# Performance work log

Hardware: AMD Instinct MI355X
Metric: run time of the kernel (lower is better)

The kernel has to match this reference:

```python
import jax, jax.numpy as jnp
import numpy as np
from jax.ops import segment_sum

N_NODES = 100000
N_EDGES = 1600000
N_GRAPHS = 128


def setup_inputs() -> dict:
    key = jax.random.key(0)
    ks = jax.random.split(key, 16)
    x = jax.random.normal(ks[0], (N_NODES, 128), dtype=jnp.float32)
    edge_index = jax.random.randint(ks[1], (2, N_EDGES), 0, N_NODES, dtype=jnp.int64)
    batch = jnp.sort(jax.random.randint(ks[2], (N_NODES,), 0, N_GRAPHS, dtype=jnp.int64))
    def glorot(k, fan_in, fan_out):
        lim = (6.0 / (fan_in + fan_out)) ** 0.5
        return jax.random.uniform(k, (fan_in, fan_out), jnp.float32, -lim, lim)
    return {
        "x": x, "edge_index": edge_index, "batch": batch,
        "W1": glorot(ks[3], 128, 64), "b1": jnp.zeros((64,), jnp.float32),
        "W2": glorot(ks[4], 64, 64),  "b2": jnp.zeros((64,), jnp.float32),
        "W3": glorot(ks[5], 64, 64),  "b3": jnp.zeros((64,), jnp.float32),
        "W4": glorot(ks[6], 64, 64),  "b4": jnp.zeros((64,), jnp.float32),
        "Wl": glorot(ks[7], 64, 1),   "bl": jnp.zeros((1,), jnp.float32),
    }


def _gcn_layer(x, row, col, norm, W, b):
    # x: [N, Cin] -> [N, Cout]; gather source feats, scale, scatter-add at target
    h = x @ W                                 # dense transform first (GCNConv order)
    msg = norm[:, None] * h[row]              # [E, Cout]
    out = segment_sum(msg, col, num_segments=N_NODES)
    return out + b


def reference(x, edge_index, batch, W1, b1, W2, b2, W3, b3, W4, b4, Wl, bl):
    row, col = edge_index[0], edge_index[1]
    # symmetric degree normalization based on in-degree of col (PyG degree(col))
    deg = segment_sum(jnp.ones((N_EDGES,), x.dtype), col, num_segments=N_NODES)
    dinv = jnp.where(deg > 0, deg ** -0.5, jnp.zeros_like(deg))
    norm = dinv[row] * dinv[col]              # [E]

    h = _gcn_layer(x, row, col, norm, W1, b1)
    h = _gcn_layer(h, row, col, norm, W2, b2)
    h = _gcn_layer(h, row, col, norm, W3, b3)
    h = _gcn_layer(h, row, col, norm, W4, b4)  # [N, 64]

    # to_dense_batch + mean(dim=1): padded zeros count, so divide by max graph size
    sums = segment_sum(h, batch, num_segments=N_GRAPHS)          # [B, 64]
    counts = segment_sum(jnp.ones((N_NODES,), h.dtype), batch, num_segments=N_GRAPHS)
    n_max = jnp.max(counts)
    pooled = sums / n_max                                        # [B, 64]
    return pooled @ Wl + bl                                      # [B, 1]
```

## Files before the change

### kernel.cpp

```cpp
#include <hip/hip_runtime.h>
#include <hip/hip_bf16.h>
#include <hip/hip_fp16.h>

#define N_NODES 100000
#define N_EDGES 1600000
#define N_GRAPHS 128

#define BSH 9
#define BNODES 512
#define NB 196
#define CAP 12288
#define BLK 512
#define EPB (N_EDGES / BLK)
#define RECMAX 10240

#define SPLIT 4

typedef __attribute__((ext_vector_type(8))) _Float16 v8h;
typedef __attribute__((ext_vector_type(4))) float v4f;


__global__ __launch_bounds__(256) void k_hist(const int* __restrict__ col,
                                              int* __restrict__ hist_t) {
    __shared__ int h[NB];
    const int t = threadIdx.x, b = blockIdx.x;
    for (int i = t; i < NB; i += 256) h[i] = 0;
    __syncthreads();
    const int e0 = b * EPB;
    for (int i = t; i < EPB; i += 256) atomicAdd(&h[col[e0 + i] >> BSH], 1);
    __syncthreads();
    for (int i = t; i < NB; i += 256) hist_t[i * BLK + b] = h[i];
}

__global__ __launch_bounds__(512) void k_cursors(const int* __restrict__ hist_t,
                                                 int* __restrict__ cursors,
                                                 int* __restrict__ bcnt) {
    __shared__ int s[BLK];
    const int t = threadIdx.x, bin = blockIdx.x;
    const int v = hist_t[bin * BLK + t];
    s[t] = v; __syncthreads();
    for (int off = 1; off < BLK; off <<= 1) {
        int a = (t >= off) ? s[t - off] : 0;
        __syncthreads(); s[t] += a; __syncthreads();
    }
    cursors[bin * BLK + t] = bin * CAP + s[t] - v;
    if (t == BLK - 1) bcnt[bin] = s[t];
}

__global__ __launch_bounds__(256) void k_mid(const int* __restrict__ row,
                                             const int* __restrict__ col,
                                             const int* __restrict__ cursors,
                                             int* __restrict__ bedges) {
    __shared__ int cur[NB];
    const int t = threadIdx.x, b = blockIdx.x;
    for (int i = t; i < NB; i += 256) cur[i] = cursors[i * BLK + b];
    __syncthreads();
    const int e0 = b * EPB;
    for (int i = t; i < EPB; i += 256) {
        const int c = col[e0 + i];
        const int r = row[e0 + i];
        const int pos = atomicAdd(&cur[c >> BSH], 1);
        bedges[pos] = r | ((c & (BNODES - 1)) << 17);
    }
}

__global__ __launch_bounds__(512) void k_build(const int* __restrict__ bedges,
                                               const int* __restrict__ bcnt,
                                               int* __restrict__ csr,
                                               int* __restrict__ offs,
                                               int* __restrict__ deg_c,
                                               float* __restrict__ dinv) {
    __shared__ int rec[RECMAX];
    __shared__ int deg[BNODES];
    __shared__ int offx[BNODES];
    __shared__ int cur[BNODES];
    const int t = threadIdx.x, bin = blockIdx.x;
    const int base = bin * CAP;
    const int cnt = bcnt[bin];
    const int vb = bin << BSH;
    const int nn = min(BNODES, N_NODES - vb);
    for (int i = t; i < cnt; i += 512) rec[i] = bedges[base + i];
    deg[t] = 0;
    __syncthreads();
    for (int i = t; i < cnt; i += 512) atomicAdd(&deg[(rec[i] >> 17) & (BNODES - 1)], 1);
    __syncthreads();
    const int d = (t < nn) ? deg[t] : 0;
    const int pd = (d + 7) & ~7;
    offx[t] = pd; __syncthreads();
    for (int off = 1; off < BNODES; off <<= 1) {
        int a = (t >= off) ? offx[t - off] : 0;
        __syncthreads(); offx[t] += a; __syncthreads();
    }
    const int myoff = offx[t] - pd;
    cur[t] = myoff;
    if (t < nn) {
        offs[vb + t] = base + myoff;
        deg_c[vb + t] = d;
        dinv[vb + t] = (d > 0) ? rsqrtf((float)d) : 0.0f;
        for (int j = d; j < pd; j++) csr[base + myoff + j] = N_NODES;
    }
    __syncthreads();
    for (int i = t; i < cnt; i += 512) {
        const int r = rec[i];
        const int pos = atomicAdd(&cur[(r >> 17) & (BNODES - 1)], 1);
        csr[base + pos] = r & 0x1FFFF;
    }
}


template <int CIN>
__global__ __launch_bounds__(256) void k_gemm(const float* __restrict__ X,
                                              const float* __restrict__ W,
                                              const float* __restrict__ dinv,
                                              __half* __restrict__ H16) {
    constexpr int SA = 72;
    constexpr int SB = 72;
    __shared__ __align__(16) _Float16 sA[128 * SA];
    __shared__ __align__(16) _Float16 sBh[64 * SB];
    __shared__ __align__(16) _Float16 sBl[64 * SB];
    const int t = threadIdx.x;
    const int w = t >> 6, lane = t & 63;
    const int quad = lane >> 4, l16 = lane & 15;
    const int nb = blockIdx.x * 128;

    v4f acc[2][4] = {};

    for (int k0 = 0; k0 < CIN; k0 += 64) {
        if (k0) __syncthreads();
        for (int i = t; i < 64 * 16; i += 256) {
            const int k = i >> 4, c4 = (i & 15) * 4;
            const float4 wv = *reinterpret_cast<const float4*>(W + (size_t)(k0 + k) * 64 + c4);
            const float wf[4] = {wv.x, wv.y, wv.z, wv.w};
            #pragma unroll
            for (int j = 0; j < 4; j++) {
                const _Float16 hi = (_Float16)wf[j];
                sBh[(c4 + j) * SB + k] = hi;
                sBl[(c4 + j) * SB + k] = (_Float16)(wf[j] - (float)hi);
            }
        }
        for (int i = t; i < 128 * 16; i += 256) {
            const int node = i >> 4, k4 = (i & 15) * 4;
            const int gn = nb + node;
            float4 v = make_float4(0.f, 0.f, 0.f, 0.f);
            if (gn < N_NODES)
                v = *reinterpret_cast<const float4*>(X + (size_t)gn * CIN + k0 + k4);
            _Float16* d = &sA[node * SA + k4];
            d[0] = (_Float16)v.x; d[1] = (_Float16)v.y;
            d[2] = (_Float16)v.z; d[3] = (_Float16)v.w;
        }
        __syncthreads();

        #pragma unroll
        for (int kt = 0; kt < 2; kt++) {
            const int kb = kt * 32 + quad * 8;
            v8h afr[2], bh[4], bl[4];
            #pragma unroll
            for (int mt = 0; mt < 2; mt++)
                afr[mt] = *reinterpret_cast<const v8h*>(&sA[(w * 32 + mt * 16 + l16) * SA + kb]);
            #pragma unroll
            for (int nt = 0; nt < 4; nt++) {
                bh[nt] = *reinterpret_cast<const v8h*>(&sBh[(nt * 16 + l16) * SB + kb]);
                bl[nt] = *reinterpret_cast<const v8h*>(&sBl[(nt * 16 + l16) * SB + kb]);
            }
            #pragma unroll
            for (int mt = 0; mt < 2; mt++)
                #pragma unroll
                for (int nt = 0; nt < 4; nt++) {
                    acc[mt][nt] = __builtin_amdgcn_mfma_f32_16x16x32_f16(afr[mt], bh[nt], acc[mt][nt], 0, 0, 0);
                    acc[mt][nt] = __builtin_amdgcn_mfma_f32_16x16x32_f16(afr[mt], bl[nt], acc[mt][nt], 0, 0, 0);
                }
        }
    }

    #pragma unroll
    for (int mt = 0; mt < 2; mt++) {
        #pragma unroll
        for (int reg = 0; reg < 4; reg++) {
            const int node = nb + w * 32 + mt * 16 + quad * 4 + reg;
            if (node < N_NODES) {
                const float dv = dinv[node];
                #pragma unroll
                for (int nt = 0; nt < 4; nt++)
                    H16[(size_t)node * 64 + nt * 16 + l16] =
                        __float2half(acc[mt][nt][reg] * dv);
            }
        }
    }
}


__global__ __launch_bounds__(256) void k_prop(const __half* __restrict__ Hin,
                                              const int* __restrict__ csr,
                                              const int* __restrict__ offs,
                                              const int* __restrict__ deg_c,
                                              const float* __restrict__ dinv,
                                              const float* __restrict__ bias,
                                              float* __restrict__ Hout) {
    const int wave = threadIdx.x >> 6, lane = threadIdx.x & 63;
    const int half = lane >> 5;
    const int c2 = lane & 31;
    const int v = (blockIdx.x * 4 + wave) * 2 + half;
    const int start = offs[v];
    const int cntp = (deg_c[v] + 7) & ~7;
    const int* ep = csr + start;
    const __half* hb = Hin + c2 * 2;
    float ax = 0.f, ay = 0.f;
    for (int j = 0; j < cntp; j += 8) {
        const int4 q0 = *reinterpret_cast<const int4*>(ep + j);
        const int4 q1 = *reinterpret_cast<const int4*>(ep + j + 4);
        const float2 f0 = __half22float2(*reinterpret_cast<const __half2*>(hb + (size_t)q0.x * 64));
        const float2 f1 = __half22float2(*reinterpret_cast<const __half2*>(hb + (size_t)q0.y * 64));
        const float2 f2 = __half22float2(*reinterpret_cast<const __half2*>(hb + (size_t)q0.z * 64));
        const float2 f3 = __half22float2(*reinterpret_cast<const __half2*>(hb + (size_t)q0.w * 64));
        const float2 f4 = __half22float2(*reinterpret_cast<const __half2*>(hb + (size_t)q1.x * 64));
        const float2 f5 = __half22float2(*reinterpret_cast<const __half2*>(hb + (size_t)q1.y * 64));
        const float2 f6 = __half22float2(*reinterpret_cast<const __half2*>(hb + (size_t)q1.z * 64));
        const float2 f7 = __half22float2(*reinterpret_cast<const __half2*>(hb + (size_t)q1.w * 64));
        ax += ((f0.x + f1.x) + (f2.x + f3.x)) + ((f4.x + f5.x) + (f6.x + f7.x));
        ay += ((f0.y + f1.y) + (f2.y + f3.y)) + ((f4.y + f5.y) + (f6.y + f7.y));
    }
    const float dv = dinv[v];
    float2 o;
    o.x = dv * ax + bias[c2 * 2];
    o.y = dv * ay + bias[c2 * 2 + 1];
    *reinterpret_cast<float2*>(Hout + (size_t)v * 64 + c2 * 2) = o;
}


__global__ __launch_bounds__(256) void k_pool(const float* __restrict__ H,
                                              const int* __restrict__ batch,
                                              float* __restrict__ partial) {
    const int g = blockIdx.x >> 2;
    const int s = blockIdx.x & (SPLIT - 1);
    int lo = 0, hi = N_NODES;
    while (lo < hi) { int m = (lo + hi) >> 1; if (batch[m] < g) lo = m + 1; else hi = m; }
    const int a = lo;
    lo = 0; hi = N_NODES;
    while (lo < hi) { int m = (lo + hi) >> 1; if (batch[m] < g + 1) lo = m + 1; else hi = m; }
    const int b = lo;

    const int wave = threadIdx.x >> 6, lane = threadIdx.x & 63;
    const int lane16 = s * 4 + wave;
    float ac0 = 0.f, ac1 = 0.f, ac2 = 0.f, ac3 = 0.f;
    int v = a + lane16;
    for (; v + 48 < b; v += 64) {
        ac0 += H[(size_t)v * 64 + lane];
        ac1 += H[(size_t)(v + 16) * 64 + lane];
        ac2 += H[(size_t)(v + 32) * 64 + lane];
        ac3 += H[(size_t)(v + 48) * 64 + lane];
    }
    for (; v < b; v += 16) ac0 += H[(size_t)v * 64 + lane];
    const float acc = (ac0 + ac1) + (ac2 + ac3);

    __shared__ float red[4][64];
    red[wave][lane] = acc;
    __syncthreads();
    if (wave == 0) {
        const float r = (red[0][lane] + red[1][lane]) + (red[2][lane] + red[3][lane]);
        partial[((size_t)s * N_GRAPHS + g) * 64 + lane] = r;
    }
}

__global__ void k_final(const float* __restrict__ partial, const int* __restrict__ batch,
                        const float* __restrict__ Wl, const float* __restrict__ bl,
                        float* __restrict__ out) {
    __shared__ int scnt[128];
    int t = threadIdx.x;
    int lo = 0, hi = N_NODES;
    while (lo < hi) { int mid = (lo + hi) >> 1; if (batch[mid] < t) lo = mid + 1; else hi = mid; }
    int a = lo;
    lo = 0; hi = N_NODES;
    while (lo < hi) { int mid = (lo + hi) >> 1; if (batch[mid] < t + 1) lo = mid + 1; else hi = mid; }
    scnt[t] = lo - a;
    __syncthreads();
    for (int off = 64; off > 0; off >>= 1) {
        if (t < off) scnt[t] = max(scnt[t], scnt[t + off]);
        __syncthreads();
    }
    const float nmax = (float)scnt[0];
    float s = 0.f;
    for (int c = 0; c < 64; c++) {
        float g = 0.f;
        #pragma unroll
        for (int p = 0; p < SPLIT; p++)
            g += partial[((size_t)p * N_GRAPHS + t) * 64 + c];
        s += g * Wl[c];
    }
    out[t] = s / nmax + bl[0];
}


extern "C" void kernel_launch(void* const* d_in, const int* in_sizes, int n_in,
                              void* d_out, int out_size, void* d_ws, size_t ws_size,
                              hipStream_t stream) {
    const float* x    = (const float*)d_in[0];
    const int*   ei   = (const int*)d_in[1];
    const int*   batch= (const int*)d_in[2];
    const float* W1 = (const float*)d_in[3];  const float* b1 = (const float*)d_in[4];
    const float* W2 = (const float*)d_in[5];  const float* b2 = (const float*)d_in[6];
    const float* W3 = (const float*)d_in[7];  const float* b3 = (const float*)d_in[8];
    const float* W4 = (const float*)d_in[9];  const float* b4 = (const float*)d_in[10];
    const float* Wl = (const float*)d_in[11]; const float* bl = (const float*)d_in[12];
    float* out = (float*)d_out;

    const int* row = ei;
    const int* col = ei + N_EDGES;

    char* ws = (char*)d_ws;
    size_t off = 0;
    auto alloc = [&](size_t bytes) {
        void* p = ws + off;
        off = (off + bytes + 255) & ~(size_t)255;
        return p;
    };
    int*    hist_t  = (int*)alloc((size_t)NB * BLK * 4);
    int*    cursors = (int*)alloc((size_t)NB * BLK * 4);
    int*    bcnt    = (int*)alloc(NB * 4);
    int*    bedges  = (int*)alloc((size_t)NB * CAP * 4);
    int*    csr     = bedges;
    int*    offs    = (int*)alloc(N_NODES * 4);
    int*    deg_c   = (int*)alloc(N_NODES * 4);
    float*  dinv    = (float*)alloc(N_NODES * 4);
    __half* h16     = (__half*)alloc((size_t)(N_NODES + 1) * 64 * 2);
    float*  h_b     = (float*)alloc((size_t)N_NODES * 64 * 4);
    float*  partial = (float*)alloc((size_t)SPLIT * N_GRAPHS * 64 * 4);

    hipMemsetAsync(h16 + (size_t)N_NODES * 64, 0, 64 * 2, stream);

    k_hist<<<BLK, 256, 0, stream>>>(col, hist_t);
    k_cursors<<<NB, 512, 0, stream>>>(hist_t, cursors, bcnt);
    k_mid<<<BLK, 256, 0, stream>>>(row, col, cursors, bedges);
    k_build<<<NB, 512, 0, stream>>>(bedges, bcnt, csr, offs, deg_c, dinv);

    const int GB = (N_NODES + 127) / 128;
    const int PB = N_NODES / 8;

    k_gemm<128><<<GB, 256, 0, stream>>>(x, W1, dinv, h16);
    k_prop<<<PB, 256, 0, stream>>>(h16, csr, offs, deg_c, dinv, b1, h_b);
    k_gemm<64><<<GB, 256, 0, stream>>>(h_b, W2, dinv, h16);
    k_prop<<<PB, 256, 0, stream>>>(h16, csr, offs, deg_c, dinv, b2, h_b);
    k_gemm<64><<<GB, 256, 0, stream>>>(h_b, W3, dinv, h16);
    k_prop<<<PB, 256, 0, stream>>>(h16, csr, offs, deg_c, dinv, b3, h_b);
    k_gemm<64><<<GB, 256, 0, stream>>>(h_b, W4, dinv, h16);
    k_prop<<<PB, 256, 0, stream>>>(h16, csr, offs, deg_c, dinv, b4, h_b);

    k_pool<<<N_GRAPHS * SPLIT, 256, 0, stream>>>(h_b, batch, partial);
    k_final<<<1, 128, 0, stream>>>(partial, batch, Wl, bl, out);
}
```

Baseline: 367.3 us.

## Store intermediate layer outputs in fp16 and widen prop gathers to 4 channels

The propagation kernel now has each lane gather 4 fp16 channels (8-byte loads) with 16 lanes per node and 4 nodes per wave, instead of 2 channels with 32 lanes per node. Intermediate layer outputs are written as fp16 and read directly by the next GEMM, which skips the fp32 write/read and the conversion step. Only the last layer still writes fp32 for pooling. This halves the intermediate activation traffic and cuts the number of gather instructions, at the cost of extra fp16 rounding of the activations between layers.

```diff
diff --git a/kernel.cpp b/kernel.cpp
--- a/kernel.cpp
+++ b/kernel.cpp
@@ -108,8 +108,8 @@
 }
 
 
-template <int CIN>
-__global__ __launch_bounds__(256) void k_gemm(const float* __restrict__ X,
+template <int CIN, typename TIN>
+__global__ __launch_bounds__(256) void k_gemm(const TIN* __restrict__ X,
                                               const float* __restrict__ W,
                                               const float* __restrict__ dinv,
                                               __half* __restrict__ H16) {
@@ -138,15 +138,26 @@
                 sBl[(c4 + j) * SB + k] = (_Float16)(wf[j] - (float)hi);
             }
         }
-        for (int i = t; i < 128 * 16; i += 256) {
-            const int node = i >> 4, k4 = (i & 15) * 4;
-            const int gn = nb + node;
-            float4 v = make_float4(0.f, 0.f, 0.f, 0.f);
-            if (gn < N_NODES)
-                v = *reinterpret_cast<const float4*>(X + (size_t)gn * CIN + k0 + k4);
-            _Float16* d = &sA[node * SA + k4];
-            d[0] = (_Float16)v.x; d[1] = (_Float16)v.y;
-            d[2] = (_Float16)v.z; d[3] = (_Float16)v.w;
+        if constexpr (sizeof(TIN) == 4) {
+            for (int i = t; i < 128 * 16; i += 256) {
+                const int node = i >> 4, k4 = (i & 15) * 4;
+                const int gn = nb + node;
+                float4 v = make_float4(0.f, 0.f, 0.f, 0.f);
+                if (gn < N_NODES)
+                    v = *reinterpret_cast<const float4*>((const float*)X + (size_t)gn * CIN + k0 + k4);
+                _Float16* d = &sA[node * SA + k4];
+                d[0] = (_Float16)v.x; d[1] = (_Float16)v.y;
+                d[2] = (_Float16)v.z; d[3] = (_Float16)v.w;
+            }
+        } else {
+            for (int i = t; i < 128 * 8; i += 256) {
+                const int node = i >> 3, k8 = (i & 7) * 8;
+                const int gn = nb + node;
+                int4 v = make_int4(0, 0, 0, 0);
+                if (gn < N_NODES)
+                    v = *reinterpret_cast<const int4*>((const __half*)X + (size_t)gn * CIN + k0 + k8);
+                *reinterpret_cast<int4*>(&sA[node * SA + k8]) = v;
+            }
         }
         __syncthreads();
 
@@ -189,41 +200,55 @@
 }
 
 
+template <typename TOUT>
 __global__ __launch_bounds__(256) void k_prop(const __half* __restrict__ Hin,
                                               const int* __restrict__ csr,
                                               const int* __restrict__ offs,
                                               const int* __restrict__ deg_c,
                                               const float* __restrict__ dinv,
                                               const float* __restrict__ bias,
-                                              float* __restrict__ Hout) {
+                                              TOUT* __restrict__ Hout) {
     const int wave = threadIdx.x >> 6, lane = threadIdx.x & 63;
-    const int half = lane >> 5;
-    const int c2 = lane & 31;
-    const int v = (blockIdx.x * 4 + wave) * 2 + half;
+    const int quad = lane >> 4;
+    const int l = lane & 15;
+    const int v = blockIdx.x * 16 + wave * 4 + quad;
     const int start = offs[v];
-    const int cntp = (deg_c[v] + 7) & ~7;
+    const int cp = (deg_c[v] + 7) & ~7;
     const int* ep = csr + start;
-    const __half* hb = Hin + c2 * 2;
-    float ax = 0.f, ay = 0.f;
-    for (int j = 0; j < cntp; j += 8) {
+    const __half* hb = Hin + l * 4;
+    float a0 = 0.f, a1 = 0.f, a2 = 0.f, a3 = 0.f;
+    for (int j = 0; j < cp; j += 8) {
         const int4 q0 = *reinterpret_cast<const int4*>(ep + j);
         const int4 q1 = *reinterpret_cast<const int4*>(ep + j + 4);
-        const float2 f0 = __half22float2(*reinterpret_cast<const __half2*>(hb + (size_t)q0.x * 64));
-        const float2 f1 = __half22float2(*reinterpret_cast<const __half2*>(hb + (size_t)q0.y * 64));
-        const float2 f2 = __half22float2(*reinterpret_cast<const __half2*>(hb + (size_t)q0.z * 64));
-        const float2 f3 = __half22float2(*reinterpret_cast<const __half2*>(hb + (size_t)q0.w * 64));
-        const float2 f4 = __half22float2(*reinterpret_cast<const __half2*>(hb + (size_t)q1.x * 64));
-        const float2 f5 = __half22float2(*reinterpret_cast<const __half2*>(hb + (size_t)q1.y * 64));
-        const float2 f6 = __half22float2(*reinterpret_cast<const __half2*>(hb + (size_t)q1.z * 64));
-        const float2 f7 = __half22float2(*reinterpret_cast<const __half2*>(hb + (size_t)q1.w * 64));
-        ax += ((f0.x + f1.x) + (f2.x + f3.x)) + ((f4.x + f5.x) + (f6.x + f7.x));
-        ay += ((f0.y + f1.y) + (f2.y + f3.y)) + ((f4.y + f5.y) + (f6.y + f7.y));
+        const int2 r0 = *reinterpret_cast<const int2*>(hb + (size_t)q0.x * 64);
+        const int2 r1 = *reinterpret_cast<const int2*>(hb + (size_t)q0.y * 64);
+        const int2 r2 = *reinterpret_cast<const int2*>(hb + (size_t)q0.z * 64);
+        const int2 r3 = *reinterpret_cast<const int2*>(hb + (size_t)q0.w * 64);
+        const int2 r4 = *reinterpret_cast<const int2*>(hb + (size_t)q1.x * 64);
+        const int2 r5 = *reinterpret_cast<const int2*>(hb + (size_t)q1.y * 64);
+        const int2 r6 = *reinterpret_cast<const int2*>(hb + (size_t)q1.z * 64);
+        const int2 r7 = *reinterpret_cast<const int2*>(hb + (size_t)q1.w * 64);
+        #define ACC(r) { \
+            const float2 u = __half22float2(*reinterpret_cast<const __half2*>(&r.x)); \
+            const float2 w = __half22float2(*reinterpret_cast<const __half2*>(&r.y)); \
+            a0 += u.x; a1 += u.y; a2 += w.x; a3 += w.y; }
+        ACC(r0) ACC(r1) ACC(r2) ACC(r3) ACC(r4) ACC(r5) ACC(r6) ACC(r7)
+        #undef ACC
     }
     const float dv = dinv[v];
-    float2 o;
-    o.x = dv * ax + bias[c2 * 2];
-    o.y = dv * ay + bias[c2 * 2 + 1];
-    *reinterpret_cast<float2*>(Hout + (size_t)v * 64 + c2 * 2) = o;
+    const float4 bs = *reinterpret_cast<const float4*>(bias + l * 4);
+    const float o0 = dv * a0 + bs.x, o1 = dv * a1 + bs.y;
+    const float o2 = dv * a2 + bs.z, o3 = dv * a3 + bs.w;
+    if constexpr (sizeof(TOUT) == 2) {
+        __half2 h[2];
+        h[0] = __floats2half2_rn(o0, o1);
+        h[1] = __floats2half2_rn(o2, o3);
+        *reinterpret_cast<int2*>((__half*)Hout + (size_t)v * 64 + l * 4) =
+            *reinterpret_cast<const int2*>(h);
+    } else {
+        float4 o; o.x = o0; o.y = o1; o.z = o2; o.w = o3;
+        *reinterpret_cast<float4*>((float*)Hout + (size_t)v * 64 + l * 4) = o;
+    }
 }
 
 
@@ -322,6 +347,7 @@
     int*    deg_c   = (int*)alloc(N_NODES * 4);
     float*  dinv    = (float*)alloc(N_NODES * 4);
     __half* h16     = (__half*)alloc((size_t)(N_NODES + 1) * 64 * 2);
+    __half* h_c     = (__half*)alloc((size_t)N_NODES * 64 * 2);
     float*  h_b     = (float*)alloc((size_t)N_NODES * 64 * 4);
     float*  partial = (float*)alloc((size_t)SPLIT * N_GRAPHS * 64 * 4);
 
@@ -333,16 +359,16 @@
     k_build<<<NB, 512, 0, stream>>>(bedges, bcnt, csr, offs, deg_c, dinv);
 
     const int GB = (N_NODES + 127) / 128;
-    const int PB = N_NODES / 8;
-
-    k_gemm<128><<<GB, 256, 0, stream>>>(x, W1, dinv, h16);
-    k_prop<<<PB, 256, 0, stream>>>(h16, csr, offs, deg_c, dinv, b1, h_b);
-    k_gemm<64><<<GB, 256, 0, stream>>>(h_b, W2, dinv, h16);
-    k_prop<<<PB, 256, 0, stream>>>(h16, csr, offs, deg_c, dinv, b2, h_b);
-    k_gemm<64><<<GB, 256, 0, stream>>>(h_b, W3, dinv, h16);
-    k_prop<<<PB, 256, 0, stream>>>(h16, csr, offs, deg_c, dinv, b3, h_b);
-    k_gemm<64><<<GB, 256, 0, stream>>>(h_b, W4, dinv, h16);
-    k_prop<<<PB, 256, 0, stream>>>(h16, csr, offs, deg_c, dinv, b4, h_b);
+    const int PB = N_NODES / 16;
+
+    k_gemm<128, float><<<GB, 256, 0, stream>>>(x, W1, dinv, h16);
+    k_prop<__half><<<PB, 256, 0, stream>>>(h16, csr, offs, deg_c, dinv, b1, h_c);
+    k_gemm<64, __half><<<GB, 256, 0, stream>>>(h_c, W2, dinv, h16);
+    k_prop<__half><<<PB, 256, 0, stream>>>(h16, csr, offs, deg_c, dinv, b2, h_c);
+    k_gemm<64, __half><<<GB, 256, 0, stream>>>(h_c, W3, dinv, h16);
+    k_prop<__half><<<PB, 256, 0, stream>>>(h16, csr, offs, deg_c, dinv, b3, h_c);
+    k_gemm<64, __half><<<GB, 256, 0, stream>>>(h_c, W4, dinv, h16);
+    k_prop<float><<<PB, 256, 0, stream>>>(h16, csr, offs, deg_c, dinv, b4, h_b);
 
     k_pool<<<N_GRAPHS * SPLIT, 256, 0, stream>>>(h_b, batch, partial);
     k_final<<<1, 128, 0, stream>>>(partial, batch, Wl, bl, out);
```

After: 360.5 us. Within noise of the previous version (-1.8%).
